# Optimization experiments

Hardware: AMD Instinct MI355X
Metric: run time of the kernel (lower is better)

Reference implementation:

```python
import jax, jax.numpy as jnp
import numpy as np

E, D, H, K, CH = 32, 512, 512, 4, 32  # n_sources, input_dim, hidden_dim, sparse_topk, confidence hidden
B = 2048
EPS = 1e-6

def setup_inputs() -> dict:
    key = jax.random.key(0)
    ks = jax.random.split(key, 8)
    init = lambda k, shape, fan_in: (jax.random.normal(k, shape, jnp.float32) / np.sqrt(fan_in)).astype(jnp.float32)
    return {
        "x":   jax.random.normal(ks[0], (B, D), jnp.float32),
        # per-expert transform MLPs (stacked over experts)
        "W1":  init(ks[1], (E, D, H), D), "b1": jnp.zeros((E, H), jnp.float32),
        "W2":  init(ks[2], (E, H, D), H), "b2": jnp.zeros((E, D), jnp.float32),
        # gating network
        "Wg1": init(ks[3], (D, H), D),    "bg1": jnp.zeros((H,), jnp.float32),
        "Wg2": init(ks[4], (H, E), H),    "bg2": jnp.zeros((E,), jnp.float32),
        # per-expert confidence nets
        "Wc1": init(ks[5], (E, D, CH), D), "bc1": jnp.zeros((E, CH), jnp.float32),
        "Wc2": init(ks[6], (E, CH, 1), CH), "bc2": jnp.zeros((E, 1), jnp.float32),
    }

def reference(x, W1, b1, W2, b2, Wg1, bg1, Wg2, bg2, Wc1, bc1, Wc2, bc2):
    # gate: softmax over experts, then top-k selection per token
    logits = jax.nn.relu(x @ Wg1 + bg1) @ Wg2 + bg2          # [B, E]
    weights = jax.nn.softmax(logits, axis=-1)                # [B, E]
    _, topi = jax.lax.top_k(weights, K)                      # [B, K] distinct expert ids

    # scan over experts, accumulating weighted-sum numerator and denominator.
    # out = sum_sel (w*c*o) / (sum_sel (w*c) + eps)  ==  torch's normalize-then-combine.
    def body(carry, packed):
        num, den = carry
        w1, bb1, w2, bb2, wc1, bbc1, wc2, bbc2, e = packed
        o = jax.nn.relu(x @ w1 + bb1) @ w2 + bb2             # [B, D] expert output
        c = jax.nn.sigmoid(jax.nn.relu(o @ wc1 + bbc1) @ wc2 + bbc2)[:, 0]  # [B]
        sel = jnp.any(topi == e, axis=1)                     # [B] token routed to expert e?
        cw = weights[:, e] * sel.astype(x.dtype) * c         # [B] gate-weight * confidence
        return (num + cw[:, None] * o, den + cw), None

    init = (jnp.zeros_like(x), jnp.zeros((x.shape[0],), x.dtype))
    (num, den), _ = jax.lax.scan(
        body, init,
        (W1, b1, W2, b2, Wc1, bc1, Wc2, bc2, jnp.arange(E, dtype=topi.dtype)))
    out = num / (den[:, None] + EPS)                         # [B, D]
    return out
```

## Files before the change

### kernel.cpp

```cpp
#include <hip/hip_runtime.h>
#include <hip/hip_bf16.h>

#define BT 2048
#define DD 512
#define HH 512
#define EE 32
#define KK 4
#define CHN 32
#define MAXCH 160

#define NB_CVT 512
#define NB_TRWC 256
#define NB_TRW 2112
#define NB_PREP (NB_CVT + NB_TRWC + NB_TRW)

typedef unsigned int u32;
typedef unsigned short u16;
typedef __attribute__((ext_vector_type(8))) short short8;
typedef __attribute__((ext_vector_type(4))) float f32x4;
typedef __attribute__((ext_vector_type(2))) u32 u32x2;
typedef __attribute__((ext_vector_type(4))) u32 u32x4;

__device__ inline u16 f2bf(float f) {
  u32 u = __builtin_bit_cast(u32, f);
  u32 r = (u + 0x7FFFu + ((u >> 16) & 1u)) >> 16;
  return (u16)r;
}
__device__ inline float bf16f(u16 b) {
  u32 u = ((u32)b) << 16;
  return __builtin_bit_cast(float, u);
}
__device__ inline u32 pack2bf(float a, float b) {
  return (u32)f2bf(a) | ((u32)f2bf(b) << 16);
}
__device__ inline void gload_lds16(const u32* g, u32* l) {
  __builtin_amdgcn_global_load_lds((const __attribute__((address_space(1))) u32*)g,
                                   (__attribute__((address_space(3))) u32*)l, 16, 0, 0);
}

__global__ __launch_bounds__(256)
void k_prep(const float* __restrict__ x, const float* __restrict__ W1,
            const float* __restrict__ W2, const float* __restrict__ Wc1,
            const float* __restrict__ Wg1,
            u16* __restrict__ xh, u16* __restrict__ xl,
            u32* __restrict__ img, u32* __restrict__ img_c) {
  const int bx = blockIdx.x;
  const int tid = threadIdx.x;
  if (bx < NB_CVT) {
    int gid = bx * 256 + tid;
    const float4* src = reinterpret_cast<const float4*>(x) + (size_t)gid * 2;
    float4 a = src[0], b = src[1];
    u32x4 hi = { pack2bf(a.x, a.y), pack2bf(a.z, a.w),
                 pack2bf(b.x, b.y), pack2bf(b.z, b.w) };
    float lx0 = a.x - bf16f(f2bf(a.x)), lx1 = a.y - bf16f(f2bf(a.y));
    float lx2 = a.z - bf16f(f2bf(a.z)), lx3 = a.w - bf16f(f2bf(a.w));
    float lx4 = b.x - bf16f(f2bf(b.x)), lx5 = b.y - bf16f(f2bf(b.y));
    float lx6 = b.z - bf16f(f2bf(b.z)), lx7 = b.w - bf16f(f2bf(b.w));
    u32x4 lo = { pack2bf(lx0, lx1), pack2bf(lx2, lx3),
                 pack2bf(lx4, lx5), pack2bf(lx6, lx7) };
    reinterpret_cast<u32x4*>(xh)[gid] = hi;
    reinterpret_cast<u32x4*>(xl)[gid] = lo;
  } else if (bx < NB_CVT + NB_TRWC) {
    int idx = (bx - NB_CVT) * 2 + (tid >> 7);
    int e = idx >> 4, s = idx & 15;
    int t127 = tid & 127;
    int q = t127 >> 5, col = t127 & 31;
    const float* W = Wc1 + (size_t)e * DD * CHN;
    float v[8];
#pragma unroll
    for (int j = 0; j < 8; ++j)
      v[j] = W[(size_t)(s * 32 + q * 8 + j) * CHN + col];
    u32x4 fr = { pack2bf(v[0], v[1]), pack2bf(v[2], v[3]),
                 pack2bf(v[4], v[5]), pack2bf(v[6], v[7]) };
    *reinterpret_cast<u32x4*>(img_c + ((size_t)e * 16 + s) * 512 + q * 128 + col * 4) = fr;
  } else {
    int u = bx - (NB_CVT + NB_TRWC);
    int z = u >> 5;
    int s = (u >> 1) & 15;
    int n = (u & 1) * 256 + tid;
    const float* W = (z < EE) ? (W1 + (size_t)z * DD * HH)
                   : (z < 2 * EE) ? (W2 + (size_t)(z - EE) * HH * DD)
                   : Wg1;
    float v[32];
#pragma unroll
    for (int k = 0; k < 32; k++)
      v[k] = W[(size_t)(s * 32 + k) * 512 + n];
    if (z == 65) {
#pragma unroll
      for (int k = 0; k < 32; k++)
        v[k] = v[k] - bf16f(f2bf(v[k]));
    }
    int nc = n >> 7, coll = n & 127;
    u32* ob = img + ((size_t)(z * 4 + nc) * 16 + s) * 2048 + coll * 4;
#pragma unroll
    for (int g = 0; g < 4; g++) {
      u32x4 fr = { pack2bf(v[g * 8 + 0], v[g * 8 + 1]),
                   pack2bf(v[g * 8 + 2], v[g * 8 + 3]),
                   pack2bf(v[g * 8 + 4], v[g * 8 + 5]),
                   pack2bf(v[g * 8 + 6], v[g * 8 + 7]) };
      *reinterpret_cast<u32x4*>(ob + g * 512) = fr;
    }
  }
}

__global__ __launch_bounds__(256)
void k_gate_mfma(const u16* __restrict__ xh, const u16* __restrict__ xl,
                 const u32* __restrict__ img, const float* __restrict__ bg1,
                 float* __restrict__ h) {
  __shared__ u32 stg[2][2][1024];
  const int chunk = blockIdx.x;
  const int hc = blockIdx.y;
  const int tid = threadIdx.x;
  const int w = tid >> 6, lane = tid & 63;
  const int l15 = lane & 15, q = lane >> 4;
  const int wm = w & 1, wn = w >> 1;
  const int nc = hc >> 1, co = (hc & 1) * 64;
  const u32* imgh = img + ((size_t)(64 * 4 + nc) * 16) * 2048;
  const u32* imgl = img + ((size_t)(65 * 4 + nc) * 16) * 2048;
  const int sq = tid >> 6, scol = tid & 63;
  auto stage = [&](int s, int b) {
    gload_lds16(imgh + s * 2048 + sq * 512 + (co + scol) * 4, stg[b][0] + tid * 4);
    gload_lds16(imgl + s * 2048 + sq * 512 + (co + scol) * 4, stg[b][1] + tid * 4);
  };
  const int t0 = chunk * 64 + wn * 32 + l15;
  const int t1 = t0 + 16;
  auto ldb = [&](const u16* src, int t, int s) {
    return *reinterpret_cast<const short8*>(src + (size_t)t * 512 + s * 32 + q * 8);
  };

  f32x4 acc[2][2];
#pragma unroll
  for (int a = 0; a < 2; a++)
#pragma unroll
    for (int b = 0; b < 2; b++) acc[a][b] = {0.f, 0.f, 0.f, 0.f};

  stage(0, 0);
  short8 bh[2], bl[2];
  bh[0] = ldb(xh, t0, 0); bh[1] = ldb(xh, t1, 0);
  bl[0] = ldb(xl, t0, 0); bl[1] = ldb(xl, t1, 0);
  __syncthreads();

  for (int s = 0; s < 16; ++s) {
    const u32* ch = stg[s & 1][0];
    const u32* cl = stg[s & 1][1];
    short8 nh[2], nl[2];
    if (s < 15) {
      stage(s + 1, (s + 1) & 1);
      nh[0] = ldb(xh, t0, s + 1); nh[1] = ldb(xh, t1, s + 1);
      nl[0] = ldb(xl, t0, s + 1); nl[1] = ldb(xl, t1, s + 1);
    }
#pragma unroll
    for (int mf = 0; mf < 2; ++mf) {
      int col = wm * 32 + mf * 16 + l15;
      short8 ah = *reinterpret_cast<const short8*>(ch + q * 256 + col * 4);
      short8 al = *reinterpret_cast<const short8*>(cl + q * 256 + col * 4);
#pragma unroll
      for (int nf = 0; nf < 2; ++nf) {
        acc[mf][nf] = __builtin_amdgcn_mfma_f32_16x16x32_bf16(ah, bh[nf], acc[mf][nf], 0, 0, 0);
        acc[mf][nf] = __builtin_amdgcn_mfma_f32_16x16x32_bf16(ah, bl[nf], acc[mf][nf], 0, 0, 0);
        acc[mf][nf] = __builtin_amdgcn_mfma_f32_16x16x32_bf16(al, bh[nf], acc[mf][nf], 0, 0, 0);
        acc[mf][nf] = __builtin_amdgcn_mfma_f32_16x16x32_bf16(al, bl[nf], acc[mf][nf], 0, 0, 0);
      }
    }
    __syncthreads();
    if (s < 15) {
      bh[0] = nh[0]; bh[1] = nh[1];
      bl[0] = nl[0]; bl[1] = nl[1];
    }
  }

#pragma unroll
  for (int mf = 0; mf < 2; ++mf) {
    int hcol = hc * 64 + wm * 32 + mf * 16 + q * 4;
    float4 bb = *reinterpret_cast<const float4*>(&bg1[hcol]);
#pragma unroll
    for (int nf = 0; nf < 2; ++nf) {
      int t = chunk * 64 + wn * 32 + nf * 16 + l15;
      float4 o;
      o.x = fmaxf(acc[mf][nf].x + bb.x, 0.f);
      o.y = fmaxf(acc[mf][nf].y + bb.y, 0.f);
      o.z = fmaxf(acc[mf][nf].z + bb.z, 0.f);
      o.w = fmaxf(acc[mf][nf].w + bb.w, 0.f);
      *reinterpret_cast<float4*>(&h[(size_t)t * HH + hcol]) = o;
    }
  }
}

__global__ __launch_bounds__(256)
void k_gate_route(const float* __restrict__ h, const float* __restrict__ Wg2,
                  const float* __restrict__ bg2, float* __restrict__ wts,
                  int* __restrict__ topi) {
  __shared__ float wg2s[HH * EE];
  __shared__ float hb[8][HH];
  const int tid = threadIdx.x;
  const int t0 = blockIdx.x * 8;
#pragma unroll
  for (int i = 0; i < 16; ++i) {
    int idx = tid + i * 256;
    reinterpret_cast<float4*>(wg2s)[idx] =
        reinterpret_cast<const float4*>(Wg2)[idx];
  }
  for (int idx = tid; idx < 8 * 128; idx += 256) {
    int m = idx >> 7, j = idx & 127;
    *reinterpret_cast<float4*>(&hb[m][4 * j]) =
        *reinterpret_cast<const float4*>(&h[(size_t)(t0 + m) * HH + 4 * j]);
  }
  __syncthreads();
  const int lane = tid & 63, wv = tid >> 6;
  const int e = lane & 31, th = lane >> 5;
  const int lt = wv * 2 + th;
  const int t = t0 + lt;
  float ac[4] = {0.f, 0.f, 0.f, 0.f};
  for (int k0 = 0; k0 < HH; k0 += 8) {
    float4 h0 = *reinterpret_cast<const float4*>(&hb[lt][k0]);
    float4 h1 = *reinterpret_cast<const float4*>(&hb[lt][k0 + 4]);
    float hv[8] = {h0.x, h0.y, h0.z, h0.w, h1.x, h1.y, h1.z, h1.w};
#pragma unroll
    for (int u = 0; u < 8; ++u)
      ac[u & 3] = fmaf(hv[u], wg2s[(k0 + u) * EE + e], ac[u & 3]);
  }
  float logit = ((ac[0] + ac[1]) + (ac[2] + ac[3])) + bg2[e];
  float mx = logit;
#pragma unroll
  for (int m = 16; m >= 1; m >>= 1) mx = fmaxf(mx, __shfl_xor(mx, m, 32));
  float ex = expf(logit - mx);
  float sm = ex;
#pragma unroll
  for (int m = 16; m >= 1; m >>= 1) sm += __shfl_xor(sm, m, 32);
  float w = ex / sm;
  wts[(size_t)t * EE + e] = w;
  float wcur = w;
  for (int j = 0; j < KK; j++) {
    float v = wcur;
    int vi = e;
#pragma unroll
    for (int m = 16; m >= 1; m >>= 1) {
      float ov = __shfl_xor(v, m, 32);
      int oi = __shfl_xor(vi, m, 32);
      if (ov > v || (ov == v && oi < vi)) { v = ov; vi = oi; }
    }
    if (e == 0) topi[(t << 2) | j] = vi;
    if (e == vi) wcur = -1.f;
  }
}

__global__ __launch_bounds__(1024)
void k_build(const int* __restrict__ topi, int* __restrict__ cnt,
             int* __restrict__ tlist, int* __restrict__ chunk2e,
             int* __restrict__ chunkloc) {
  __shared__ int lcnt[EE];
  const int tid = threadIdx.x;
  if (tid < EE) lcnt[tid] = 0;
  __syncthreads();
  for (int i = tid; i < BT * KK; i += 1024) {
    int e = topi[i];
    int pos = atomicAdd(&lcnt[e], 1);
    tlist[(size_t)e * BT + pos] = i;
  }
  __syncthreads();
  if (tid < EE) {
    int e = tid;
    cnt[e] = lcnt[e];
    int off = 0, tot = 0;
    for (int j = 0; j < EE; ++j) {
      int nj = (lcnt[j] + 63) >> 6;
      if (j < e) off += nj;
      tot += nj;
    }
    int myn = (lcnt[e] + 63) >> 6;
    for (int j = 0; j < myn; ++j) {
      chunk2e[off + j] = e; chunkloc[off + j] = j;
    }
    for (int idx = tot + e; idx < MAXCH; idx += EE) {
      chunk2e[idx] = -1; chunkloc[idx] = 0;
    }
  }
}

__device__ inline int remap_chunk(int bx) {
  return (bx & 7) * (MAXCH / 8) + (bx >> 3);
}

__global__ __launch_bounds__(256)
void k_gemm1(const u16* __restrict__ xb, const u32* __restrict__ img,
             const float* __restrict__ b1, const int* __restrict__ cnt,
             const int* __restrict__ tlist, const int* __restrict__ chunk2e,
             const int* __restrict__ chunkloc, u32* __restrict__ hid) {
  __shared__ u32 stg[2][4096];
  __shared__ int tkl[64];
  const int c = remap_chunk(blockIdx.x);
  const int e = chunk2e[c];
  if (e < 0) return;
  const int hc = blockIdx.y;
  const int loc = chunkloc[c];
  const int nt = cnt[e];
  const int tid = threadIdx.x;
  const int w = tid >> 6, lane = tid & 63;
  const int l15 = lane & 15, q = lane >> 4;
  const int wm = w & 1, wn = w >> 1;

  const u32* imgb = img + ((size_t)(e * 4 + hc) * 16) * 2048;
  auto stage = [&](int st, u32* dst) {
    const u32* src = imgb + st * 4096;
#pragma unroll
    for (int i = 0; i < 4; i++)
      gload_lds16(src + tid * 4 + i * 1024, dst + tid * 4 + i * 1024);
  };

  stage(0, stg[0]);
  if (tid < 64) {
    int i = min(loc * 64 + tid, nt - 1);
    tkl[tid] = tlist[(size_t)e * BT + i] >> 2;
  }
  __syncthreads();

  const int t0 = tkl[wn * 32 + l15];
  const int t1 = tkl[wn * 32 + 16 + l15];
  auto ldb = [&](int t, int st, int ss) {
    return *reinterpret_cast<const short8*>(
        xb + (size_t)t * 512 + st * 64 + ss * 32 + q * 8);
  };

  f32x4 acc[4][2];
#pragma unroll
  for (int a = 0; a < 4; a++)
#pragma unroll
    for (int b = 0; b < 2; b++) acc[a][b] = {0.f, 0.f, 0.f, 0.f};

  short8 bfr[2][2];
  bfr[0][0] = ldb(t0, 0, 0); bfr[0][1] = ldb(t0, 0, 1);
  bfr[1][0] = ldb(t1, 0, 0); bfr[1][1] = ldb(t1, 0, 1);

  for (int st = 0; st < 8; ++st) {
    const u32* cur = stg[st & 1];
    short8 nb[2][2];
    if (st < 7) {
      stage(st + 1, stg[(st + 1) & 1]);
      nb[0][0] = ldb(t0, st + 1, 0); nb[0][1] = ldb(t0, st + 1, 1);
      nb[1][0] = ldb(t1, st + 1, 0); nb[1][1] = ldb(t1, st + 1, 1);
    }
#pragma unroll
    for (int ss = 0; ss < 2; ++ss) {
#pragma unroll
      for (int mf = 0; mf < 4; ++mf) {
        int col = wm * 64 + mf * 16 + l15;
        short8 af = *reinterpret_cast<const short8*>(
            cur + ss * 2048 + q * 512 + col * 4);
        acc[mf][0] = __builtin_amdgcn_mfma_f32_16x16x32_bf16(af, bfr[0][ss], acc[mf][0], 0, 0, 0);
        acc[mf][1] = __builtin_amdgcn_mfma_f32_16x16x32_bf16(af, bfr[1][ss], acc[mf][1], 0, 0, 0);
      }
    }
    __syncthreads();
    if (st < 7) {
      bfr[0][0] = nb[0][0]; bfr[0][1] = nb[0][1];
      bfr[1][0] = nb[1][0]; bfr[1][1] = nb[1][1];
    }
  }

  const float* b1e = b1 + (size_t)e * HH;
#pragma unroll
  for (int mf = 0; mf < 4; ++mf) {
    int h0 = hc * 128 + wm * 64 + mf * 16 + q * 4;
    float4 bb = *reinterpret_cast<const float4*>(b1e + h0);
#pragma unroll
    for (int nf = 0; nf < 2; ++nf) {
      int local = wn * 32 + nf * 16 + l15;
      int prow = c * 64 + local;
      float v0 = fmaxf(acc[mf][nf].x + bb.x, 0.f);
      float v1 = fmaxf(acc[mf][nf].y + bb.y, 0.f);
      float v2 = fmaxf(acc[mf][nf].z + bb.z, 0.f);
      float v3 = fmaxf(acc[mf][nf].w + bb.w, 0.f);
      u32x2 pk = { pack2bf(v0, v1), pack2bf(v2, v3) };
      *reinterpret_cast<u32x2*>(hid + (size_t)prow * 256 + (h0 >> 1)) = pk;
    }
  }
}

__global__ __launch_bounds__(256)
void k_gemm2(const u32* __restrict__ hid, const u32* __restrict__ img,
             const float* __restrict__ b2, const int* __restrict__ cnt,
             const int* __restrict__ tlist, const int* __restrict__ chunk2e,
             const int* __restrict__ chunkloc, float* __restrict__ o_p) {
  __shared__ u32 stg[2][4096];
  __shared__ int tke[64];
  const int c = remap_chunk(blockIdx.x);
  const int e = chunk2e[c];
  if (e < 0) return;
  const int dc = blockIdx.y;
  const int loc = chunkloc[c];
  const int nt = cnt[e];
  const int tid = threadIdx.x;
  const int w = tid >> 6, lane = tid & 63;
  const int l15 = lane & 15, q = lane >> 4;
  const int wm = w & 1, wn = w >> 1;
  const int rows_c = min(64, nt - loc * 64);

  const u32* imgb = img + ((size_t)((EE + e) * 4 + dc) * 16) * 2048;
  auto stage = [&](int st, u32* dst) {
    const u32* src = imgb + st * 4096;
#pragma unroll
    for (int i = 0; i < 4; i++)
      gload_lds16(src + tid * 4 + i * 1024, dst + tid * 4 + i * 1024);
  };

  stage(0, stg[0]);
  if (tid < 64) {
    int i = min(loc * 64 + tid, nt - 1);
    tke[tid] = tlist[(size_t)e * BT + i];
  }
  __syncthreads();

  const u16* hid16 = (const u16*)hid;
  const int pr0 = c * 64 + wn * 32 + l15;
  const int pr1 = pr0 + 16;
  auto ldb = [&](int pr, int st, int ss) {
    return *reinterpret_cast<const short8*>(
        hid16 + (size_t)pr * 512 + st * 64 + ss * 32 + q * 8);
  };

  f32x4 acc[4][2];
#pragma unroll
  for (int a = 0; a < 4; a++)
#pragma unroll
    for (int b = 0; b < 2; b++) acc[a][b] = {0.f, 0.f, 0.f, 0.f};

  short8 bfr[2][2];
  bfr[0][0] = ldb(pr0, 0, 0); bfr[0][1] = ldb(pr0, 0, 1);
  bfr[1][0] = ldb(pr1, 0, 0); bfr[1][1] = ldb(pr1, 0, 1);

  for (int st = 0; st < 8; ++st) {
    const u32* cur = stg[st & 1];
    short8 nb[2][2];
    if (st < 7) {
      stage(st + 1, stg[(st + 1) & 1]);
      nb[0][0] = ldb(pr0, st + 1, 0); nb[0][1] = ldb(pr0, st + 1, 1);
      nb[1][0] = ldb(pr1, st + 1, 0); nb[1][1] = ldb(pr1, st + 1, 1);
    }
#pragma unroll
    for (int ss = 0; ss < 2; ++ss) {
#pragma unroll
      for (int mf = 0; mf < 4; ++mf) {
        int col = wm * 64 + mf * 16 + l15;
        short8 af = *reinterpret_cast<const short8*>(
            cur + ss * 2048 + q * 512 + col * 4);
        acc[mf][0] = __builtin_amdgcn_mfma_f32_16x16x32_bf16(af, bfr[0][ss], acc[mf][0], 0, 0, 0);
        acc[mf][1] = __builtin_amdgcn_mfma_f32_16x16x32_bf16(af, bfr[1][ss], acc[mf][1], 0, 0, 0);
      }
    }
    __syncthreads();
    if (st < 7) {
      bfr[0][0] = nb[0][0]; bfr[0][1] = nb[0][1];
      bfr[1][0] = nb[1][0]; bfr[1][1] = nb[1][1];
    }
  }

  const float* b2e = b2 + (size_t)e * DD;
#pragma unroll
  for (int mf = 0; mf < 4; ++mf) {
    int d0 = dc * 128 + wm * 64 + mf * 16 + q * 4;
    float4 bb = *reinterpret_cast<const float4*>(b2e + d0);
#pragma unroll
    for (int nf = 0; nf < 2; ++nf) {
      int local = wn * 32 + nf * 16 + l15;
      if (local < rows_c) {
        int ent = tke[local];
        int t = ent >> 2, sl = ent & 3;
        float4 v;
        v.x = acc[mf][nf].x + bb.x;
        v.y = acc[mf][nf].y + bb.y;
        v.z = acc[mf][nf].z + bb.z;
        v.w = acc[mf][nf].w + bb.w;
        *reinterpret_cast<float4*>(&o_p[((size_t)t * KK + sl) * DD + d0]) = v;
      }
    }
  }
}

__global__ __launch_bounds__(256)
void k_conf2(const float* __restrict__ o_p, const u32* __restrict__ img_c,
             const float* __restrict__ bc1, const float* __restrict__ Wc2,
             const float* __restrict__ bc2, const float* __restrict__ wts,
             const int* __restrict__ cnt, const int* __restrict__ tlist,
             const int* __restrict__ chunk2e, const int* __restrict__ chunkloc,
             float* __restrict__ cw) {
  __shared__ u32 stg[8192];
  __shared__ int tke[64];
  const int c = remap_chunk(blockIdx.x);
  const int e = chunk2e[c];
  if (e < 0) return;
  const int loc = chunkloc[c];
  const int nt = cnt[e];
  const int tid = threadIdx.x;
  const int w = tid >> 6, lane = tid & 63;
  const int l15 = lane & 15, q = lane >> 4;

  const u32* src = img_c + (size_t)e * 16 * 512;
#pragma unroll
  for (int i = 0; i < 8; ++i)
    gload_lds16(src + tid * 4 + i * 1024, stg + tid * 4 + i * 1024);
  if (tid < 64) {
    int i = min(loc * 64 + tid, nt - 1);
    tke[tid] = tlist[(size_t)e * BT + i];
  }
  __syncthreads();

  const int rows_c = min(64, nt - loc * 64);
  const int local = w * 16 + l15;
  const int ent = tke[local];
  const float* orow = o_p + (size_t)ent * DD;

  f32x4 acc0 = {0.f, 0.f, 0.f, 0.f}, acc1 = {0.f, 0.f, 0.f, 0.f};
#pragma unroll
  for (int st = 0; st < 16; ++st) {
    float4 f0 = *reinterpret_cast<const float4*>(orow + st * 32 + q * 8);
    float4 f1 = *reinterpret_cast<const float4*>(orow + st * 32 + q * 8 + 4);
    u32x4 bp = { pack2bf(f0.x, f0.y), pack2bf(f0.z, f0.w),
                 pack2bf(f1.x, f1.y), pack2bf(f1.z, f1.w) };
    short8 bfrag = __builtin_bit_cast(short8, bp);
    short8 af0 = *reinterpret_cast<const short8*>(
        stg + st * 512 + q * 128 + l15 * 4);
    short8 af1 = *reinterpret_cast<const short8*>(
        stg + st * 512 + q * 128 + (16 + l15) * 4);
    acc0 = __builtin_amdgcn_mfma_f32_16x16x32_bf16(af0, bfrag, acc0, 0, 0, 0);
    acc1 = __builtin_amdgcn_mfma_f32_16x16x32_bf16(af1, bfrag, acc1, 0, 0, 0);
  }

  float part = 0.f;
#pragma unroll
  for (int i = 0; i < 4; ++i) {
    int ch0 = q * 4 + i, ch1 = 16 + q * 4 + i;
    float h0 = fmaxf(acc0[i] + bc1[(size_t)e * CHN + ch0], 0.f);
    float h1 = fmaxf(acc1[i] + bc1[(size_t)e * CHN + ch1], 0.f);
    part = fmaf(h0, Wc2[(size_t)e * CHN + ch0], part);
    part = fmaf(h1, Wc2[(size_t)e * CHN + ch1], part);
  }
  part += __shfl_xor(part, 16);
  part += __shfl_xor(part, 32);
  if (q == 0 && local < rows_c) {
    float cv = 1.f / (1.f + expf(-(part + bc2[e])));
    cw[ent] = wts[(size_t)(ent >> 2) * EE + e] * cv;
  }
}

__global__ __launch_bounds__(256)
void k_combine(const float* __restrict__ o_p, const float* __restrict__ cw,
               float* __restrict__ out) {
  int gid = blockIdx.x * 256 + threadIdx.x;
  int t = gid >> 7;
  int j = gid & 127;
  float c0 = cw[t * 4 + 0], c1 = cw[t * 4 + 1];
  float c2 = cw[t * 4 + 2], c3 = cw[t * 4 + 3];
  float den = c0 + c1 + c2 + c3 + 1e-6f;
  const float4* base = reinterpret_cast<const float4*>(o_p) + (size_t)t * 4 * 128;
  float4 v0 = base[0 * 128 + j];
  float4 v1 = base[1 * 128 + j];
  float4 v2 = base[2 * 128 + j];
  float4 v3 = base[3 * 128 + j];
  float4 r;
  r.x = (c0 * v0.x + c1 * v1.x + c2 * v2.x + c3 * v3.x) / den;
  r.y = (c0 * v0.y + c1 * v1.y + c2 * v2.y + c3 * v3.y) / den;
  r.z = (c0 * v0.z + c1 * v1.z + c2 * v2.z + c3 * v3.z) / den;
  r.w = (c0 * v0.w + c1 * v1.w + c2 * v2.w + c3 * v3.w) / den;
  reinterpret_cast<float4*>(out)[gid] = r;
}

extern "C" void kernel_launch(void* const* d_in, const int* in_sizes, int n_in,
                              void* d_out, int out_size, void* d_ws, size_t ws_size,
                              hipStream_t stream) {
  const float* x   = (const float*)d_in[0];
  const float* W1  = (const float*)d_in[1];
  const float* b1  = (const float*)d_in[2];
  const float* W2  = (const float*)d_in[3];
  const float* b2  = (const float*)d_in[4];
  const float* Wg1 = (const float*)d_in[5];
  const float* bg1 = (const float*)d_in[6];
  const float* Wg2 = (const float*)d_in[7];
  const float* bg2 = (const float*)d_in[8];
  const float* Wc1 = (const float*)d_in[9];
  const float* bc1 = (const float*)d_in[10];
  const float* Wc2 = (const float*)d_in[11];
  const float* bc2 = (const float*)d_in[12];
  float* out = (float*)d_out;

  char* p = (char*)d_ws;
  u16* xh = (u16*)p;            p += (size_t)BT * DD * 2;
  u32* img = (u32*)p;           p += (size_t)66 * 4 * 16 * 2048 * 4;
  float* h_g = (float*)p;
  u16* xl = (u16*)(p + (size_t)4 * 1024 * 1024);
  u32* hid = (u32*)p;           p += (size_t)MAXCH * 64 * DD * 2;
  float* wts = (float*)p;       p += (size_t)BT * EE * 4;
  float* cw  = (float*)p;       p += (size_t)BT * KK * 4;
  float* o_p = (float*)p;       p += (size_t)BT * KK * DD * 4;
  int* cnt = (int*)p;           p += 256;
  int* tlist = (int*)p;         p += (size_t)EE * BT * 4;
  int* chunk2e = (int*)p;       p += 1024;
  int* chunkloc = (int*)p;      p += 1024;
  u32* img_c = (u32*)p;         p += (size_t)EE * 16 * 512 * 4;
  int* topi = (int*)p;          p += (size_t)BT * KK * 4;

  k_prep<<<NB_PREP, 256, 0, stream>>>(x, W1, W2, Wc1, Wg1,
                                      xh, xl, img, img_c);
  k_gate_mfma<<<dim3(32, 8), 256, 0, stream>>>(xh, xl, img, bg1, h_g);
  k_gate_route<<<BT / 8, 256, 0, stream>>>(h_g, Wg2, bg2, wts, topi);
  k_build<<<1, 1024, 0, stream>>>(topi, cnt, tlist, chunk2e, chunkloc);
  k_gemm1<<<dim3(MAXCH, 4), 256, 0, stream>>>(xh, img, b1, cnt, tlist,
                                              chunk2e, chunkloc, hid);
  k_gemm2<<<dim3(MAXCH, 4), 256, 0, stream>>>(hid, img, b2, cnt, tlist,
                                              chunk2e, chunkloc, o_p);
  k_conf2<<<MAXCH, 256, 0, stream>>>(o_p, img_c, bc1, Wc2, bc2, wts,
                                     cnt, tlist, chunk2e, chunkloc, cw);
  k_combine<<<(BT * (DD / 4)) / 256, 256, 0, stream>>>(o_p, cw, out);
}
```

Baseline: 105.6 us.

## Compute gate logits with split-bf16 MFMA and pack Wg2 in prep

```diff
diff --git a/kernel.cpp b/kernel.cpp
--- a/kernel.cpp
+++ b/kernel.cpp
@@ -10,7 +10,7 @@
 #define MAXCH 160
 
 #define NB_CVT 512
-#define NB_TRWC 256
+#define NB_TRWC 272
 #define NB_TRW 2112
 #define NB_PREP (NB_CVT + NB_TRWC + NB_TRW)
 
@@ -41,7 +41,7 @@
 __global__ __launch_bounds__(256)
 void k_prep(const float* __restrict__ x, const float* __restrict__ W1,
             const float* __restrict__ W2, const float* __restrict__ Wc1,
-            const float* __restrict__ Wg1,
+            const float* __restrict__ Wg1, const float* __restrict__ Wg2,
             u16* __restrict__ xh, u16* __restrict__ xl,
             u32* __restrict__ img, u32* __restrict__ img_c) {
   const int bx = blockIdx.x;
@@ -65,11 +65,16 @@
     int e = idx >> 4, s = idx & 15;
     int t127 = tid & 127;
     int q = t127 >> 5, col = t127 & 31;
-    const float* W = Wc1 + (size_t)e * DD * CHN;
+    const float* W = (e < EE) ? (Wc1 + (size_t)e * DD * CHN) : Wg2;
     float v[8];
 #pragma unroll
     for (int j = 0; j < 8; ++j)
       v[j] = W[(size_t)(s * 32 + q * 8 + j) * CHN + col];
+    if (e == 33) {
+#pragma unroll
+      for (int j = 0; j < 8; ++j)
+        v[j] = v[j] - bf16f(f2bf(v[j]));
+    }
     u32x4 fr = { pack2bf(v[0], v[1]), pack2bf(v[2], v[3]),
                  pack2bf(v[4], v[5]), pack2bf(v[6], v[7]) };
     *reinterpret_cast<u32x4*>(img_c + ((size_t)e * 16 + s) * 512 + q * 128 + col * 4) = fr;
@@ -106,7 +111,7 @@
 __global__ __launch_bounds__(256)
 void k_gate_mfma(const u16* __restrict__ xh, const u16* __restrict__ xl,
                  const u32* __restrict__ img, const float* __restrict__ bg1,
-                 float* __restrict__ h) {
+                 u16* __restrict__ hh, u16* __restrict__ hl) {
   __shared__ u32 stg[2][2][1024];
   const int chunk = blockIdx.x;
   const int hc = blockIdx.y;
@@ -176,71 +181,105 @@
 #pragma unroll
     for (int nf = 0; nf < 2; ++nf) {
       int t = chunk * 64 + wn * 32 + nf * 16 + l15;
-      float4 o;
-      o.x = fmaxf(acc[mf][nf].x + bb.x, 0.f);
-      o.y = fmaxf(acc[mf][nf].y + bb.y, 0.f);
-      o.z = fmaxf(acc[mf][nf].z + bb.z, 0.f);
-      o.w = fmaxf(acc[mf][nf].w + bb.w, 0.f);
-      *reinterpret_cast<float4*>(&h[(size_t)t * HH + hcol]) = o;
+      float v0 = fmaxf(acc[mf][nf].x + bb.x, 0.f);
+      float v1 = fmaxf(acc[mf][nf].y + bb.y, 0.f);
+      float v2 = fmaxf(acc[mf][nf].z + bb.z, 0.f);
+      float v3 = fmaxf(acc[mf][nf].w + bb.w, 0.f);
+      u32x2 hi = { pack2bf(v0, v1), pack2bf(v2, v3) };
+      float r0 = v0 - bf16f(f2bf(v0)), r1 = v1 - bf16f(f2bf(v1));
+      float r2 = v2 - bf16f(f2bf(v2)), r3 = v3 - bf16f(f2bf(v3));
+      u32x2 lo = { pack2bf(r0, r1), pack2bf(r2, r3) };
+      *reinterpret_cast<u32x2*>(hh + (size_t)t * 512 + hcol) = hi;
+      *reinterpret_cast<u32x2*>(hl + (size_t)t * 512 + hcol) = lo;
     }
   }
 }
 
 __global__ __launch_bounds__(256)
-void k_gate_route(const float* __restrict__ h, const float* __restrict__ Wg2,
-                  const float* __restrict__ bg2, float* __restrict__ wts,
-                  int* __restrict__ topi) {
-  __shared__ float wg2s[HH * EE];
-  __shared__ float hb[8][HH];
+void k_route2(const u16* __restrict__ hh, const u16* __restrict__ hl,
+              const u32* __restrict__ img_c, const float* __restrict__ bg2,
+              float* __restrict__ wts, int* __restrict__ topi) {
+  __shared__ u32 sh[8192];
+  __shared__ u32 sl_[8192];
+  const int chunk = blockIdx.x;
   const int tid = threadIdx.x;
-  const int t0 = blockIdx.x * 8;
-#pragma unroll
-  for (int i = 0; i < 16; ++i) {
-    int idx = tid + i * 256;
-    reinterpret_cast<float4*>(wg2s)[idx] =
-        reinterpret_cast<const float4*>(Wg2)[idx];
-  }
-  for (int idx = tid; idx < 8 * 128; idx += 256) {
-    int m = idx >> 7, j = idx & 127;
-    *reinterpret_cast<float4*>(&hb[m][4 * j]) =
-        *reinterpret_cast<const float4*>(&h[(size_t)(t0 + m) * HH + 4 * j]);
+  const int w = tid >> 6, lane = tid & 63;
+  const int l15 = lane & 15, q = lane >> 4;
+  const u32* srch = img_c + (size_t)32 * 16 * 512;
+  const u32* srcl = img_c + (size_t)33 * 16 * 512;
+#pragma unroll
+  for (int i = 0; i < 8; ++i) {
+    gload_lds16(srch + tid * 4 + i * 1024, sh + tid * 4 + i * 1024);
+    gload_lds16(srcl + tid * 4 + i * 1024, sl_ + tid * 4 + i * 1024);
   }
   __syncthreads();
-  const int lane = tid & 63, wv = tid >> 6;
-  const int e = lane & 31, th = lane >> 5;
-  const int lt = wv * 2 + th;
-  const int t = t0 + lt;
-  float ac[4] = {0.f, 0.f, 0.f, 0.f};
-  for (int k0 = 0; k0 < HH; k0 += 8) {
-    float4 h0 = *reinterpret_cast<const float4*>(&hb[lt][k0]);
-    float4 h1 = *reinterpret_cast<const float4*>(&hb[lt][k0 + 4]);
-    float hv[8] = {h0.x, h0.y, h0.z, h0.w, h1.x, h1.y, h1.z, h1.w};
-#pragma unroll
-    for (int u = 0; u < 8; ++u)
-      ac[u & 3] = fmaf(hv[u], wg2s[(k0 + u) * EE + e], ac[u & 3]);
-  }
-  float logit = ((ac[0] + ac[1]) + (ac[2] + ac[3])) + bg2[e];
-  float mx = logit;
-#pragma unroll
-  for (int m = 16; m >= 1; m >>= 1) mx = fmaxf(mx, __shfl_xor(mx, m, 32));
-  float ex = expf(logit - mx);
-  float sm = ex;
-#pragma unroll
-  for (int m = 16; m >= 1; m >>= 1) sm += __shfl_xor(sm, m, 32);
-  float w = ex / sm;
-  wts[(size_t)t * EE + e] = w;
-  float wcur = w;
-  for (int j = 0; j < KK; j++) {
-    float v = wcur;
-    int vi = e;
-#pragma unroll
-    for (int m = 16; m >= 1; m >>= 1) {
-      float ov = __shfl_xor(v, m, 32);
-      int oi = __shfl_xor(vi, m, 32);
-      if (ov > v || (ov == v && oi < vi)) { v = ov; vi = oi; }
-    }
-    if (e == 0) topi[(t << 2) | j] = vi;
-    if (e == vi) wcur = -1.f;
+
+  const int t = chunk * 64 + w * 16 + l15;
+  const u16* rh = hh + (size_t)t * 512;
+  const u16* rl = hl + (size_t)t * 512;
+  f32x4 acc0 = {0.f, 0.f, 0.f, 0.f}, acc1 = {0.f, 0.f, 0.f, 0.f};
+#pragma unroll
+  for (int st = 0; st < 16; ++st) {
+    short8 bh = *reinterpret_cast<const short8*>(rh + st * 32 + q * 8);
+    short8 bl = *reinterpret_cast<const short8*>(rl + st * 32 + q * 8);
+    short8 ah0 = *reinterpret_cast<const short8*>(sh + st * 512 + q * 128 + l15 * 4);
+    short8 ah1 = *reinterpret_cast<const short8*>(sh + st * 512 + q * 128 + (16 + l15) * 4);
+    short8 al0 = *reinterpret_cast<const short8*>(sl_ + st * 512 + q * 128 + l15 * 4);
+    short8 al1 = *reinterpret_cast<const short8*>(sl_ + st * 512 + q * 128 + (16 + l15) * 4);
+    acc0 = __builtin_amdgcn_mfma_f32_16x16x32_bf16(ah0, bh, acc0, 0, 0, 0);
+    acc0 = __builtin_amdgcn_mfma_f32_16x16x32_bf16(ah0, bl, acc0, 0, 0, 0);
+    acc0 = __builtin_amdgcn_mfma_f32_16x16x32_bf16(al0, bh, acc0, 0, 0, 0);
+    acc0 = __builtin_amdgcn_mfma_f32_16x16x32_bf16(al0, bl, acc0, 0, 0, 0);
+    acc1 = __builtin_amdgcn_mfma_f32_16x16x32_bf16(ah1, bh, acc1, 0, 0, 0);
+    acc1 = __builtin_amdgcn_mfma_f32_16x16x32_bf16(ah1, bl, acc1, 0, 0, 0);
+    acc1 = __builtin_amdgcn_mfma_f32_16x16x32_bf16(al1, bh, acc1, 0, 0, 0);
+    acc1 = __builtin_amdgcn_mfma_f32_16x16x32_bf16(al1, bl, acc1, 0, 0, 0);
+  }
+
+  float lv[8];
+  int li[8];
+#pragma unroll
+  for (int i = 0; i < 4; ++i) {
+    li[i] = q * 4 + i;
+    lv[i] = acc0[i] + bg2[li[i]];
+    li[4 + i] = 16 + q * 4 + i;
+    lv[4 + i] = acc1[i] + bg2[li[4 + i]];
+  }
+  float mx = lv[0];
+#pragma unroll
+  for (int k = 1; k < 8; ++k) mx = fmaxf(mx, lv[k]);
+  mx = fmaxf(mx, __shfl_xor(mx, 16));
+  mx = fmaxf(mx, __shfl_xor(mx, 32));
+  float ex[8], sm = 0.f;
+#pragma unroll
+  for (int k = 0; k < 8; ++k) { ex[k] = expf(lv[k] - mx); sm += ex[k]; }
+  sm += __shfl_xor(sm, 16);
+  sm += __shfl_xor(sm, 32);
+  float inv = 1.f / sm;
+  float4 w0 = { ex[0] * inv, ex[1] * inv, ex[2] * inv, ex[3] * inv };
+  float4 w1 = { ex[4] * inv, ex[5] * inv, ex[6] * inv, ex[7] * inv };
+  *reinterpret_cast<float4*>(&wts[(size_t)t * EE + q * 4]) = w0;
+  *reinterpret_cast<float4*>(&wts[(size_t)t * EE + 16 + q * 4]) = w1;
+  unsigned used = 0;
+  for (int j = 0; j < KK; ++j) {
+    float bv = -1e30f;
+    int bi = 64;
+#pragma unroll
+    for (int k = 0; k < 8; ++k) {
+      if (!((used >> k) & 1u) && (lv[k] > bv || (lv[k] == bv && li[k] < bi))) {
+        bv = lv[k]; bi = li[k];
+      }
+    }
+#pragma unroll
+    for (int m = 16; m <= 32; m <<= 1) {
+      float ov = __shfl_xor(bv, m);
+      int oi = __shfl_xor(bi, m);
+      if (ov > bv || (ov == bv && oi < bi)) { bv = ov; bi = oi; }
+    }
+    if (q == 0) topi[(t << 2) | j] = bi;
+#pragma unroll
+    for (int k = 0; k < 8; ++k)
+      if (li[k] == bi) used |= 1u << k;
   }
 }
 
@@ -585,7 +624,8 @@
   char* p = (char*)d_ws;
   u16* xh = (u16*)p;            p += (size_t)BT * DD * 2;
   u32* img = (u32*)p;           p += (size_t)66 * 4 * 16 * 2048 * 4;
-  float* h_g = (float*)p;
+  u16* hh = (u16*)p;
+  u16* hl = (u16*)(p + (size_t)2 * 1024 * 1024);
   u16* xl = (u16*)(p + (size_t)4 * 1024 * 1024);
   u32* hid = (u32*)p;           p += (size_t)MAXCH * 64 * DD * 2;
   float* wts = (float*)p;       p += (size_t)BT * EE * 4;
@@ -595,13 +635,13 @@
   int* tlist = (int*)p;         p += (size_t)EE * BT * 4;
   int* chunk2e = (int*)p;       p += 1024;
   int* chunkloc = (int*)p;      p += 1024;
-  u32* img_c = (u32*)p;         p += (size_t)EE * 16 * 512 * 4;
+  u32* img_c = (u32*)p;         p += (size_t)34 * 16 * 512 * 4;
   int* topi = (int*)p;          p += (size_t)BT * KK * 4;
 
-  k_prep<<<NB_PREP, 256, 0, stream>>>(x, W1, W2, Wc1, Wg1,
+  k_prep<<<NB_PREP, 256, 0, stream>>>(x, W1, W2, Wc1, Wg1, Wg2,
                                       xh, xl, img, img_c);
-  k_gate_mfma<<<dim3(32, 8), 256, 0, stream>>>(xh, xl, img, bg1, h_g);
-  k_gate_route<<<BT / 8, 256, 0, stream>>>(h_g, Wg2, bg2, wts, topi);
+  k_gate_mfma<<<dim3(32, 8), 256, 0, stream>>>(xh, xl, img, bg1, hh, hl);
+  k_route2<<<32, 256, 0, stream>>>(hh, hl, img_c, bg2, wts, topi);
   k_build<<<1, 1024, 0, stream>>>(topi, cnt, tlist, chunk2e, chunkloc);
   k_gemm1<<<dim3(MAXCH, 4), 256, 0, stream>>>(xh, img, b1, cnt, tlist,
                                               chunk2e, chunkloc, hid);
```

After: 106.1 us. Within noise of the previous version (+0.5%).
